# Optimization experiments

Measured on AMD Instinct MI355X. Metric: run time of the kernel, lower is better.

## Reference

```python
import jax, jax.numpy as jnp
import numpy as np


def setup_inputs() -> dict:
    key = jax.random.key(0)
    k1, k2 = jax.random.split(key)
    B, H, W, C = 32, 32, 32, 256
    N_EMBED = 1024
    z = jax.random.normal(k1, (B, H, W, C), dtype=jnp.float32)
    emb_weights = jax.random.normal(k2, (N_EMBED, C), dtype=jnp.float32)
    return {"z": z, "emb_weights": emb_weights}


def reference(z, emb_weights):
    # z: (B,H,W,C) -> flatten to (N, C)
    B = z.shape[0]
    C = z.shape[-1]
    z_flat = z.reshape(-1, C)  # (N, C)
    # Squared euclidean distance via ||z||^2 + ||e||^2 - 2 z.e^T
    distance = (
        jnp.sum(z_flat ** 2, axis=1, keepdims=True)          # (N, 1)
        + jnp.sum(emb_weights ** 2, axis=1)                   # (n_embed,)
        - 2.0 * jnp.dot(z_flat, emb_weights.T)                # (N, n_embed)
    )
    min_encoding_indices = jnp.argmin(distance, axis=1)       # (N,)
    z_q = emb_weights[min_encoding_indices].reshape(z.shape)  # (B,H,W,C)
    min_encoding_indices = min_encoding_indices.reshape(B, -1)
    return z_q, min_encoding_indices
```

## Files before the change

kernel.cpp:

```cpp
#include <hip/hip_runtime.h>

#define C_DIM 256
#define NCODE 1024
#define MARGIN 0.02f

typedef __bf16 bf16x8 __attribute__((ext_vector_type(8)));
typedef float f32x4 __attribute__((ext_vector_type(4)));

#define WS_ENORM 0
#define WS_META  4096
#define WS_RLIST 8192
#define WS_BP    139264
#define WS_PB    1187840
#define WS_PBI   1712128

#define GLOAD_LDS16(g, s)                                                            \
  __builtin_amdgcn_global_load_lds(                                                  \
      (const __attribute__((address_space(1))) unsigned int*)(g),                    \
      (__attribute__((address_space(3))) unsigned int*)(s), 16, 0, 0)

__device__ __forceinline__ void bf16split(float x, unsigned short& h, unsigned short& l) {
    unsigned u  = __float_as_uint(x);
    unsigned rh = (u + 0x7FFFu + ((u >> 16) & 1u)) & 0xFFFF0000u;
    float    lf = x - __uint_as_float(rh);
    unsigned ul = __float_as_uint(lf);
    h = (unsigned short)(rh >> 16);
    l = (unsigned short)((ul + 0x7FFFu + ((ul >> 16) & 1u)) >> 16);
}

__global__ __launch_bounds__(256) void prep_misc_kernel(const float* __restrict__ emb,
                                                        float* __restrict__ enorm,
                                                        unsigned* __restrict__ meta) {
    int gid = blockIdx.x * 256 + threadIdx.x;
    if (gid == 0) meta[0] = 0u;
    int row = gid >> 6, lane = gid & 63;
    float4 v = reinterpret_cast<const float4*>(emb)[(size_t)row * 64 + lane];
    float s = v.x * v.x + v.y * v.y + v.z * v.z + v.w * v.w;
    #pragma unroll
    for (int off = 32; off; off >>= 1) s += __shfl_xor(s, off, 64);
    if (lane == 0) enorm[row] = s;
}

__global__ __launch_bounds__(256) void prep_b_kernel(const float* __restrict__ emb,
                                                     unsigned short* __restrict__ bp) {
    int tid = blockIdx.x * 256 + threadIdx.x;
    int j   = tid >> 5;
    int u   = tid & 31;
    int kc  = u >> 2, lg = u & 3;
    const float* src = emb + (size_t)j * C_DIM + kc * 32 + lg * 8;
    float4 v0 = *reinterpret_cast<const float4*>(src);
    float4 v1 = *reinterpret_cast<const float4*>(src + 4);
    float vs[8] = {v0.x, v0.y, v0.z, v0.w, v1.x, v1.y, v1.z, v1.w};
    unsigned short h[8], l[8];
    #pragma unroll
    for (int k = 0; k < 8; ++k) bf16split(vs[k], h[k], l[k]);
    int chunk = j >> 5, nf = (j >> 4) & 1, lr = j & 15;
    int lane  = lg * 16 + lr;
    size_t base = (size_t)chunk * 16384 + (size_t)(nf * 8 + kc) * 512 + lane * 8;
    uint4 hp, lp;
    hp.x = (unsigned)h[0] | ((unsigned)h[1] << 16);
    hp.y = (unsigned)h[2] | ((unsigned)h[3] << 16);
    hp.z = (unsigned)h[4] | ((unsigned)h[5] << 16);
    hp.w = (unsigned)h[6] | ((unsigned)h[7] << 16);
    lp.x = (unsigned)l[0] | ((unsigned)l[1] << 16);
    lp.y = (unsigned)l[2] | ((unsigned)l[3] << 16);
    lp.z = (unsigned)l[4] | ((unsigned)l[5] << 16);
    lp.w = (unsigned)l[6] | ((unsigned)l[7] << 16);
    *reinterpret_cast<uint4*>(bp + base)             = hp;
    *reinterpret_cast<uint4*>(bp + base + 16 * 512)  = lp;
}

__global__ __launch_bounds__(512, 2) void vq_main_kernel(
    const float* __restrict__ z, const unsigned short* __restrict__ bp,
    const float* __restrict__ enorm, float2* __restrict__ pb,
    unsigned* __restrict__ pbi) {
    __shared__ alignas(16) unsigned short Bds[2][16384];
    __shared__ float en_s[512];
    __shared__ float mv1[128][2], mv2[128][2];
    __shared__ unsigned mi[128][2];

    const int t    = threadIdx.x;
    const int w    = t >> 6;
    const int lane = t & 63;
    const int lr   = lane & 15, lg = lane >> 4;
    const int wm   = w >> 1;
    const int ng   = w & 1;
    const int  nh  = blockIdx.x & 1;
    const long r0  = (long)(blockIdx.x >> 1) * 128;
    const unsigned short* bph = bp + (size_t)nh * 16 * 16384;

    #pragma unroll
    for (int round = 0; round < 4; ++round) {
        int f = round * 8 + w;
        GLOAD_LDS16(bph + (size_t)f * 512 + lane * 8, &Bds[0][f * 512]);
    }
    if (t < 512) en_s[t] = enorm[nh * 512 + t];

    bf16x8 ah[2][8], al[2][8];
    #pragma unroll
    for (int m = 0; m < 2; ++m) {
        const float* zr = z + (r0 + wm * 32 + m * 16 + lr) * C_DIM + lg * 8;
        #pragma unroll
        for (int kc = 0; kc < 8; ++kc) {
            float4 v0 = *reinterpret_cast<const float4*>(zr + kc * 32);
            float4 v1 = *reinterpret_cast<const float4*>(zr + kc * 32 + 4);
            float vs[8] = {v0.x, v0.y, v0.z, v0.w, v1.x, v1.y, v1.z, v1.w};
            unsigned short hv[8], lv[8];
            #pragma unroll
            for (int jj = 0; jj < 8; ++jj) bf16split(vs[jj], hv[jj], lv[jj]);
            unsigned hp[4] = {
                (unsigned)hv[0] | ((unsigned)hv[1] << 16), (unsigned)hv[2] | ((unsigned)hv[3] << 16),
                (unsigned)hv[4] | ((unsigned)hv[5] << 16), (unsigned)hv[6] | ((unsigned)hv[7] << 16)};
            unsigned lp[4] = {
                (unsigned)lv[0] | ((unsigned)lv[1] << 16), (unsigned)lv[2] | ((unsigned)lv[3] << 16),
                (unsigned)lv[4] | ((unsigned)lv[5] << 16), (unsigned)lv[6] | ((unsigned)lv[7] << 16)};
            ah[m][kc] = __builtin_bit_cast(bf16x8, *reinterpret_cast<uint4*>(hp));
            al[m][kc] = __builtin_bit_cast(bf16x8, *reinterpret_cast<uint4*>(lp));
        }
    }

    float b1[2][4], b2[2][4]; unsigned i1[2][4];
    #pragma unroll
    for (int m = 0; m < 2; ++m)
        #pragma unroll
        for (int r = 0; r < 4; ++r) { b1[m][r] = 3.4e38f; b2[m][r] = 3.4e38f; i1[m][r] = 0; }

    for (int c = 0; c < 16; ++c) {
        const int cur = c & 1;
        __syncthreads();
        if (c < 15) {
            const unsigned short* src = bph + (size_t)(c + 1) * 16384;
            #pragma unroll
            for (int round = 0; round < 4; ++round) {
                int f = round * 8 + w;
                GLOAD_LDS16(src + (size_t)f * 512 + lane * 8, &Bds[cur ^ 1][f * 512]);
            }
            asm volatile("s_waitcnt vmcnt(4)" ::: "memory");
        } else {
            asm volatile("s_waitcnt vmcnt(0)" ::: "memory");
        }
        __syncthreads();

        f32x4 hh0 = {0.f,0.f,0.f,0.f}, hh1 = {0.f,0.f,0.f,0.f};
        f32x4 hl0 = {0.f,0.f,0.f,0.f}, hl1 = {0.f,0.f,0.f,0.f};
        f32x4 lh0 = {0.f,0.f,0.f,0.f}, lh1 = {0.f,0.f,0.f,0.f};
        const unsigned short* bb = &Bds[cur][(ng * 8) * 512 + lane * 8];
        #pragma unroll
        for (int kc = 0; kc < 8; ++kc) {
            bf16x8 bh = *reinterpret_cast<const bf16x8*>(bb + kc * 512);
            bf16x8 bl = *reinterpret_cast<const bf16x8*>(bb + (16 + kc) * 512);
            hh0 = __builtin_amdgcn_mfma_f32_16x16x32_bf16(ah[0][kc], bh, hh0, 0, 0, 0);
            hh1 = __builtin_amdgcn_mfma_f32_16x16x32_bf16(ah[1][kc], bh, hh1, 0, 0, 0);
            lh0 = __builtin_amdgcn_mfma_f32_16x16x32_bf16(al[0][kc], bh, lh0, 0, 0, 0);
            lh1 = __builtin_amdgcn_mfma_f32_16x16x32_bf16(al[1][kc], bh, lh1, 0, 0, 0);
            hl0 = __builtin_amdgcn_mfma_f32_16x16x32_bf16(ah[0][kc], bl, hl0, 0, 0, 0);
            hl1 = __builtin_amdgcn_mfma_f32_16x16x32_bf16(ah[1][kc], bl, hl1, 0, 0, 0);
        }

        const float    en   = en_s[c * 32 + ng * 16 + lr];
        const unsigned code = (unsigned)(nh * 512 + c * 32 + ng * 16 + lr);
        #pragma unroll
        for (int r = 0; r < 4; ++r) {
            float d0 = fmaf(-2.f, hh0[r] + hl0[r] + lh0[r], en);
            if (d0 < b1[0][r]) { b2[0][r] = b1[0][r]; b1[0][r] = d0; i1[0][r] = code; }
            else if (d0 < b2[0][r]) { b2[0][r] = d0; }
            float d1 = fmaf(-2.f, hh1[r] + hl1[r] + lh1[r], en);
            if (d1 < b1[1][r]) { b2[1][r] = b1[1][r]; b1[1][r] = d1; i1[1][r] = code; }
            else if (d1 < b2[1][r]) { b2[1][r] = d1; }
        }
    }

    #pragma unroll
    for (int m = 0; m < 2; ++m)
        #pragma unroll
        for (int r = 0; r < 4; ++r) {
            float v1 = b1[m][r], v2 = b2[m][r]; unsigned j1 = i1[m][r];
            #pragma unroll
            for (int off = 8; off; off >>= 1) {
                float    ov1 = __shfl_xor(v1, off, 64);
                float    ov2 = __shfl_xor(v2, off, 64);
                unsigned oj1 = (unsigned)__shfl_xor((int)j1, off, 64);
                if (ov1 < v1 || (ov1 == v1 && oj1 < j1)) {
                    v2 = fminf(v1, ov2); v1 = ov1; j1 = oj1;
                } else {
                    v2 = fminf(v2, ov1);
                }
            }
            if (lr == 0) {
                int rowl = wm * 32 + m * 16 + lg * 4 + r;
                mv1[rowl][ng] = v1; mv2[rowl][ng] = v2; mi[rowl][ng] = j1;
            }
        }
    __syncthreads();
    if (t < 128) {
        float B1 = mv1[t][0], B2 = mv2[t][0]; unsigned I1 = mi[t][0];
        float o1 = mv1[t][1], o2 = mv2[t][1]; unsigned O1 = mi[t][1];
        if (o1 < B1 || (o1 == B1 && O1 < I1)) { B2 = fminf(B1, o2); B1 = o1; I1 = O1; }
        else                                  { B2 = fminf(B2, o1); }
        pb [(r0 + t) * 2 + nh] = make_float2(B1, B2);
        pbi[(r0 + t) * 2 + nh] = I1;
    }
}

__global__ __launch_bounds__(256) void finalize_gather_kernel(
    const float* __restrict__ emb, const float2* __restrict__ pb,
    const unsigned* __restrict__ pbi, float* __restrict__ zq,
    float* __restrict__ idx_out, unsigned* __restrict__ meta,
    unsigned* __restrict__ rlist) {
    const long row = (long)blockIdx.x * 4 + (threadIdx.x >> 6);
    const int lane = threadIdx.x & 63;
    float2   p0 = pb [row * 2 + 0], p1 = pb [row * 2 + 1];
    unsigned j0 = pbi[row * 2 + 0], j1 = pbi[row * 2 + 1];
    float B1, B2; unsigned I1;
    if (p1.x < p0.x) { B1 = p1.x; I1 = j1; B2 = fminf(p0.x, p1.y); }
    else             { B1 = p0.x; I1 = j0; B2 = fminf(p0.y, p1.x); }
    if (lane == 0) {
        idx_out[row] = (float)I1;
        if (B2 - B1 <= MARGIN) rlist[atomicAdd(meta, 1u)] = (unsigned)row;
    }
    float4 v = reinterpret_cast<const float4*>(emb)[(size_t)I1 * 64 + lane];
    reinterpret_cast<float4*>(zq)[row * 64 + lane] = v;
}

__global__ __launch_bounds__(256) void rescue_kernel(
    const float* __restrict__ z, const float* __restrict__ emb,
    const float* __restrict__ enorm, const unsigned* __restrict__ meta,
    const unsigned* __restrict__ rlist, float* __restrict__ zq,
    float* __restrict__ idx_out) {
    __shared__ float zrow[C_DIM];
    __shared__ float rd[256];
    __shared__ unsigned rix[256];
    const unsigned cnt = meta[0];
    for (unsigned li = blockIdx.x; li < cnt; li += gridDim.x) {
        unsigned row = rlist[li];
        __syncthreads();
        if (threadIdx.x < 64) {
            float4 v = reinterpret_cast<const float4*>(z)[(size_t)row * 64 + threadIdx.x];
            reinterpret_cast<float4*>(zrow)[threadIdx.x] = v;
        }
        __syncthreads();
        const int c = threadIdx.x;
        float a0 = 0.f, a1 = 0.f, a2 = 0.f, a3 = 0.f;
        const float4* zp = reinterpret_cast<const float4*>(zrow);
        const float4* e0 = reinterpret_cast<const float4*>(emb + (size_t)(c)       * C_DIM);
        const float4* e1 = reinterpret_cast<const float4*>(emb + (size_t)(c + 256) * C_DIM);
        const float4* e2 = reinterpret_cast<const float4*>(emb + (size_t)(c + 512) * C_DIM);
        const float4* e3 = reinterpret_cast<const float4*>(emb + (size_t)(c + 768) * C_DIM);
        #pragma unroll 8
        for (int k = 0; k < 64; ++k) {
            float4 z4 = zp[k];
            float4 f0 = e0[k], f1 = e1[k], f2 = e2[k], f3 = e3[k];
            a0 = fmaf(z4.x, f0.x, a0); a0 = fmaf(z4.y, f0.y, a0);
            a0 = fmaf(z4.z, f0.z, a0); a0 = fmaf(z4.w, f0.w, a0);
            a1 = fmaf(z4.x, f1.x, a1); a1 = fmaf(z4.y, f1.y, a1);
            a1 = fmaf(z4.z, f1.z, a1); a1 = fmaf(z4.w, f1.w, a1);
            a2 = fmaf(z4.x, f2.x, a2); a2 = fmaf(z4.y, f2.y, a2);
            a2 = fmaf(z4.z, f2.z, a2); a2 = fmaf(z4.w, f2.w, a2);
            a3 = fmaf(z4.x, f3.x, a3); a3 = fmaf(z4.y, f3.y, a3);
            a3 = fmaf(z4.z, f3.z, a3); a3 = fmaf(z4.w, f3.w, a3);
        }
        float d0 = fmaf(-2.f, a0, enorm[c]);
        float d1 = fmaf(-2.f, a1, enorm[c + 256]);
        float d2 = fmaf(-2.f, a2, enorm[c + 512]);
        float d3 = fmaf(-2.f, a3, enorm[c + 768]);
        float bd = d0; unsigned bi = (unsigned)c;
        if (d1 < bd) { bd = d1; bi = (unsigned)(c + 256); }
        if (d2 < bd) { bd = d2; bi = (unsigned)(c + 512); }
        if (d3 < bd) { bd = d3; bi = (unsigned)(c + 768); }
        rd[threadIdx.x] = bd; rix[threadIdx.x] = bi;
        __syncthreads();
        for (int s = 128; s; s >>= 1) {
            if (threadIdx.x < (unsigned)s) {
                float od = rd[threadIdx.x + s]; unsigned oi = rix[threadIdx.x + s];
                if (od < rd[threadIdx.x] ||
                    (od == rd[threadIdx.x] && oi < rix[threadIdx.x])) {
                    rd[threadIdx.x] = od; rix[threadIdx.x] = oi;
                }
            }
            __syncthreads();
        }
        unsigned code = rix[0];
        if (threadIdx.x < 64) {
            float4 v = reinterpret_cast<const float4*>(emb)[(size_t)code * 64 + threadIdx.x];
            reinterpret_cast<float4*>(zq)[(size_t)row * 64 + threadIdx.x] = v;
        }
        if (threadIdx.x == 0) idx_out[row] = (float)code;
    }
}

extern "C" void kernel_launch(void* const* d_in, const int* in_sizes, int n_in,
                              void* d_out, int out_size, void* d_ws, size_t ws_size,
                              hipStream_t stream) {
    const float* z   = (const float*)d_in[0];
    const float* emb = (const float*)d_in[1];
    const int n = in_sizes[0] / C_DIM;

    float* zq      = (float*)d_out;
    float* idx_out = zq + (size_t)n * C_DIM;

    char* ws = (char*)d_ws;
    float*          enorm = (float*)(ws + WS_ENORM);
    unsigned*       meta  = (unsigned*)(ws + WS_META);
    unsigned*       rlist = (unsigned*)(ws + WS_RLIST);
    unsigned short* bp    = (unsigned short*)(ws + WS_BP);
    float2*         pb    = (float2*)(ws + WS_PB);
    unsigned*       pbi   = (unsigned*)(ws + WS_PBI);

    prep_misc_kernel<<<256, 256, 0, stream>>>(emb, enorm, meta);
    prep_b_kernel<<<128, 256, 0, stream>>>(emb, bp);
    vq_main_kernel<<<(n / 128) * 2, 512, 0, stream>>>(z, bp, enorm, pb, pbi);
    finalize_gather_kernel<<<n / 4, 256, 0, stream>>>(emb, pb, pbi, zq, idx_out,
                                                      meta, rlist);
    rescue_kernel<<<256, 256, 0, stream>>>(z, emb, enorm, meta, rlist, zq, idx_out);
}
```

Baseline: 149.3 us.

## Split VQ search into bf16 coarse pass, split-bf16 refine pass, then fp32 rescue

The main pass now computes distances with a single bf16 MFMA product instead of the three-term hi/lo split, cutting MFMA work by about two thirds and halving B traffic. Each wave now owns all 32 codes of a chunk, and a 4-deep prefetch ring replaces double buffering. Rows whose top-two gap falls under a wider margin are re-scored over all codes by a new stage-2 kernel that uses the split-bf16 precision. Rows that remain ambiguous go to the existing fp32 rescue kernel. The risk is that the wider margin sends many rows to stage 2 and adds a kernel launch.

Result: slower. 219.2 us (+46.9%).

```diff
diff --git a/kernel.cpp b/kernel.cpp
--- a/kernel.cpp
+++ b/kernel.cpp
@@ -2,37 +2,44 @@
 
 #define C_DIM 256
 #define NCODE 1024
-#define MARGIN 0.02f
+#define MARGIN1 0.35f
+#define MARGIN2 0.02f
 
 typedef __bf16 bf16x8 __attribute__((ext_vector_type(8)));
 typedef float f32x4 __attribute__((ext_vector_type(4)));
 
-#define WS_ENORM 0
-#define WS_META  4096
-#define WS_RLIST 8192
-#define WS_BP    139264
-#define WS_PB    1187840
-#define WS_PBI   1712128
+#define WS_ENORM  0
+#define WS_META   4096
+#define WS_RLIST  8192
+#define WS_RLIST2 139264
+#define WS_BP     270336
+#define WS_PB     1318912
+#define WS_PBI    1843200
+
+#define BP_LO_OFF 262144
 
 #define GLOAD_LDS16(g, s)                                                            \
   __builtin_amdgcn_global_load_lds(                                                  \
       (const __attribute__((address_space(1))) unsigned int*)(g),                    \
       (__attribute__((address_space(3))) unsigned int*)(s), 16, 0, 0)
 
+__device__ __forceinline__ unsigned short bf16rne(float x) {
+    unsigned u = __float_as_uint(x);
+    return (unsigned short)((u + 0x7FFFu + ((u >> 16) & 1u)) >> 16);
+}
 __device__ __forceinline__ void bf16split(float x, unsigned short& h, unsigned short& l) {
     unsigned u  = __float_as_uint(x);
     unsigned rh = (u + 0x7FFFu + ((u >> 16) & 1u)) & 0xFFFF0000u;
     float    lf = x - __uint_as_float(rh);
-    unsigned ul = __float_as_uint(lf);
     h = (unsigned short)(rh >> 16);
-    l = (unsigned short)((ul + 0x7FFFu + ((ul >> 16) & 1u)) >> 16);
+    l = bf16rne(lf);
 }
 
 __global__ __launch_bounds__(256) void prep_misc_kernel(const float* __restrict__ emb,
                                                         float* __restrict__ enorm,
                                                         unsigned* __restrict__ meta) {
     int gid = blockIdx.x * 256 + threadIdx.x;
-    if (gid == 0) meta[0] = 0u;
+    if (gid < 2) meta[gid] = 0u;
     int row = gid >> 6, lane = gid & 63;
     float4 v = reinterpret_cast<const float4*>(emb)[(size_t)row * 64 + lane];
     float s = v.x * v.x + v.y * v.y + v.z * v.z + v.w * v.w;
@@ -56,7 +63,7 @@
     for (int k = 0; k < 8; ++k) bf16split(vs[k], h[k], l[k]);
     int chunk = j >> 5, nf = (j >> 4) & 1, lr = j & 15;
     int lane  = lg * 16 + lr;
-    size_t base = (size_t)chunk * 16384 + (size_t)(nf * 8 + kc) * 512 + lane * 8;
+    size_t base = (size_t)chunk * 8192 + (size_t)(nf * 8 + kc) * 512 + lane * 8;
     uint4 hp, lp;
     hp.x = (unsigned)h[0] | ((unsigned)h[1] << 16);
     hp.y = (unsigned)h[2] | ((unsigned)h[3] << 16);
@@ -67,57 +74,53 @@
     lp.z = (unsigned)l[4] | ((unsigned)l[5] << 16);
     lp.w = (unsigned)l[6] | ((unsigned)l[7] << 16);
     *reinterpret_cast<uint4*>(bp + base)             = hp;
-    *reinterpret_cast<uint4*>(bp + base + 16 * 512)  = lp;
-}
-
-__global__ __launch_bounds__(512, 2) void vq_main_kernel(
+    *reinterpret_cast<uint4*>(bp + BP_LO_OFF + base) = lp;
+}
+
+__global__ __launch_bounds__(256, 2) void vq_stage1_kernel(
     const float* __restrict__ z, const unsigned short* __restrict__ bp,
     const float* __restrict__ enorm, float2* __restrict__ pb,
     unsigned* __restrict__ pbi) {
-    __shared__ alignas(16) unsigned short Bds[2][16384];
+    __shared__ unsigned short Bds[4][8192];
     __shared__ float en_s[512];
-    __shared__ float mv1[128][2], mv2[128][2];
-    __shared__ unsigned mi[128][2];
-
-    const int t    = threadIdx.x;
-    const int w    = t >> 6;
-    const int lane = t & 63;
-    const int lr   = lane & 15, lg = lane >> 4;
-    const int wm   = w >> 1;
-    const int ng   = w & 1;
-    const int  nh  = blockIdx.x & 1;
-    const long r0  = (long)(blockIdx.x >> 1) * 128;
-    const unsigned short* bph = bp + (size_t)nh * 16 * 16384;
-
-    #pragma unroll
-    for (int round = 0; round < 4; ++round) {
-        int f = round * 8 + w;
-        GLOAD_LDS16(bph + (size_t)f * 512 + lane * 8, &Bds[0][f * 512]);
-    }
-    if (t < 512) en_s[t] = enorm[nh * 512 + t];
-
-    bf16x8 ah[2][8], al[2][8];
+
+    const int t = threadIdx.x;
+    const int w = t >> 6, lane = t & 63;
+    const int lr = lane & 15, lg = lane >> 4;
+    const int nh = blockIdx.x & 1;
+    const long r0 = (long)(blockIdx.x >> 1) * 128 + w * 32;
+    const unsigned short* bsrc = bp + (size_t)(nh * 16) * 8192 + lane * 8;
+
+    en_s[t]       = enorm[nh * 512 + t];
+    en_s[t + 256] = enorm[nh * 512 + 256 + t];
+
+    bf16x8 ah[2][8];
     #pragma unroll
     for (int m = 0; m < 2; ++m) {
-        const float* zr = z + (r0 + wm * 32 + m * 16 + lr) * C_DIM + lg * 8;
+        const float* zr = z + (r0 + m * 16 + lr) * C_DIM + lg * 8;
         #pragma unroll
         for (int kc = 0; kc < 8; ++kc) {
             float4 v0 = *reinterpret_cast<const float4*>(zr + kc * 32);
             float4 v1 = *reinterpret_cast<const float4*>(zr + kc * 32 + 4);
             float vs[8] = {v0.x, v0.y, v0.z, v0.w, v1.x, v1.y, v1.z, v1.w};
-            unsigned short hv[8], lv[8];
-            #pragma unroll
-            for (int jj = 0; jj < 8; ++jj) bf16split(vs[jj], hv[jj], lv[jj]);
-            unsigned hp[4] = {
-                (unsigned)hv[0] | ((unsigned)hv[1] << 16), (unsigned)hv[2] | ((unsigned)hv[3] << 16),
-                (unsigned)hv[4] | ((unsigned)hv[5] << 16), (unsigned)hv[6] | ((unsigned)hv[7] << 16)};
-            unsigned lp[4] = {
-                (unsigned)lv[0] | ((unsigned)lv[1] << 16), (unsigned)lv[2] | ((unsigned)lv[3] << 16),
-                (unsigned)lv[4] | ((unsigned)lv[5] << 16), (unsigned)lv[6] | ((unsigned)lv[7] << 16)};
+            unsigned hp[4];
+            #pragma unroll
+            for (int p = 0; p < 4; ++p)
+                hp[p] = (unsigned)bf16rne(vs[2 * p]) |
+                        ((unsigned)bf16rne(vs[2 * p + 1]) << 16);
             ah[m][kc] = __builtin_bit_cast(bf16x8, *reinterpret_cast<uint4*>(hp));
-            al[m][kc] = __builtin_bit_cast(bf16x8, *reinterpret_cast<uint4*>(lp));
         }
     }
+    __syncthreads();
+
+#define STG1(c) {                                                       \
+    unsigned short* db = &Bds[(c) & 3][0];                              \
+    const unsigned short* gs = bsrc + (size_t)(c) * 8192;               \
+    _Pragma("unroll") for (int rd = 0; rd < 4; ++rd) {                  \
+        int s_ = rd * 4 + w;                                            \
+        GLOAD_LDS16(gs + s_ * 512, db + s_ * 512); } }
+
+    STG1(0); STG1(1); STG1(2);
 
     float b1[2][4], b2[2][4]; unsigned i1[2][4];
     #pragma unroll
@@ -125,50 +128,47 @@
         #pragma unroll
         for (int r = 0; r < 4; ++r) { b1[m][r] = 3.4e38f; b2[m][r] = 3.4e38f; i1[m][r] = 0; }
 
+    #pragma unroll 1
     for (int c = 0; c < 16; ++c) {
-        const int cur = c & 1;
-        __syncthreads();
-        if (c < 15) {
-            const unsigned short* src = bph + (size_t)(c + 1) * 16384;
-            #pragma unroll
-            for (int round = 0; round < 4; ++round) {
-                int f = round * 8 + w;
-                GLOAD_LDS16(src + (size_t)f * 512 + lane * 8, &Bds[cur ^ 1][f * 512]);
-            }
-            asm volatile("s_waitcnt vmcnt(4)" ::: "memory");
-        } else {
-            asm volatile("s_waitcnt vmcnt(0)" ::: "memory");
-        }
-        __syncthreads();
-
-        f32x4 hh0 = {0.f,0.f,0.f,0.f}, hh1 = {0.f,0.f,0.f,0.f};
-        f32x4 hl0 = {0.f,0.f,0.f,0.f}, hl1 = {0.f,0.f,0.f,0.f};
-        f32x4 lh0 = {0.f,0.f,0.f,0.f}, lh1 = {0.f,0.f,0.f,0.f};
-        const unsigned short* bb = &Bds[cur][(ng * 8) * 512 + lane * 8];
+        if (c < 13) {
+            STG1(c + 3);
+            asm volatile("s_waitcnt vmcnt(12)" ::: "memory");
+        } else if (c == 13) { asm volatile("s_waitcnt vmcnt(8)" ::: "memory"); }
+        else if (c == 14)   { asm volatile("s_waitcnt vmcnt(4)" ::: "memory"); }
+        else                { asm volatile("s_waitcnt vmcnt(0)" ::: "memory"); }
+        __builtin_amdgcn_s_barrier();
+
+        f32x4 a00 = {0.f,0.f,0.f,0.f}, a01 = {0.f,0.f,0.f,0.f};
+        f32x4 a10 = {0.f,0.f,0.f,0.f}, a11 = {0.f,0.f,0.f,0.f};
+        const unsigned short* bb = &Bds[c & 3][lane * 8];
         #pragma unroll
         for (int kc = 0; kc < 8; ++kc) {
-            bf16x8 bh = *reinterpret_cast<const bf16x8*>(bb + kc * 512);
-            bf16x8 bl = *reinterpret_cast<const bf16x8*>(bb + (16 + kc) * 512);
-            hh0 = __builtin_amdgcn_mfma_f32_16x16x32_bf16(ah[0][kc], bh, hh0, 0, 0, 0);
-            hh1 = __builtin_amdgcn_mfma_f32_16x16x32_bf16(ah[1][kc], bh, hh1, 0, 0, 0);
-            lh0 = __builtin_amdgcn_mfma_f32_16x16x32_bf16(al[0][kc], bh, lh0, 0, 0, 0);
-            lh1 = __builtin_amdgcn_mfma_f32_16x16x32_bf16(al[1][kc], bh, lh1, 0, 0, 0);
-            hl0 = __builtin_amdgcn_mfma_f32_16x16x32_bf16(ah[0][kc], bl, hl0, 0, 0, 0);
-            hl1 = __builtin_amdgcn_mfma_f32_16x16x32_bf16(ah[1][kc], bl, hl1, 0, 0, 0);
-        }
-
-        const float    en   = en_s[c * 32 + ng * 16 + lr];
-        const unsigned code = (unsigned)(nh * 512 + c * 32 + ng * 16 + lr);
-        #pragma unroll
-        for (int r = 0; r < 4; ++r) {
-            float d0 = fmaf(-2.f, hh0[r] + hl0[r] + lh0[r], en);
-            if (d0 < b1[0][r]) { b2[0][r] = b1[0][r]; b1[0][r] = d0; i1[0][r] = code; }
-            else if (d0 < b2[0][r]) { b2[0][r] = d0; }
-            float d1 = fmaf(-2.f, hh1[r] + hl1[r] + lh1[r], en);
-            if (d1 < b1[1][r]) { b2[1][r] = b1[1][r]; b1[1][r] = d1; i1[1][r] = code; }
-            else if (d1 < b2[1][r]) { b2[1][r] = d1; }
-        }
+            bf16x8 bh0 = *reinterpret_cast<const bf16x8*>(bb + kc * 512);
+            bf16x8 bh1 = *reinterpret_cast<const bf16x8*>(bb + (8 + kc) * 512);
+            a00 = __builtin_amdgcn_mfma_f32_16x16x32_bf16(ah[0][kc], bh0, a00, 0, 0, 0);
+            a10 = __builtin_amdgcn_mfma_f32_16x16x32_bf16(ah[1][kc], bh0, a10, 0, 0, 0);
+            a01 = __builtin_amdgcn_mfma_f32_16x16x32_bf16(ah[0][kc], bh1, a01, 0, 0, 0);
+            a11 = __builtin_amdgcn_mfma_f32_16x16x32_bf16(ah[1][kc], bh1, a11, 0, 0, 0);
+        }
+
+        #pragma unroll
+        for (int nf = 0; nf < 2; ++nf) {
+            const int cl = c * 32 + nf * 16 + lr;
+            const float en = en_s[cl];
+            const unsigned code = (unsigned)(nh * 512 + cl);
+            #pragma unroll
+            for (int r = 0; r < 4; ++r) {
+                float d0 = fmaf(-2.f, (nf ? a01[r] : a00[r]), en);
+                if (d0 < b1[0][r]) { b2[0][r] = b1[0][r]; b1[0][r] = d0; i1[0][r] = code; }
+                else if (d0 < b2[0][r]) { b2[0][r] = d0; }
+                float d1 = fmaf(-2.f, (nf ? a11[r] : a10[r]), en);
+                if (d1 < b1[1][r]) { b2[1][r] = b1[1][r]; b1[1][r] = d1; i1[1][r] = code; }
+                else if (d1 < b2[1][r]) { b2[1][r] = d1; }
+            }
+        }
+        __builtin_amdgcn_s_barrier();
     }
+#undef STG1
 
     #pragma unroll
     for (int m = 0; m < 2; ++m)
@@ -187,19 +187,11 @@
                 }
             }
             if (lr == 0) {
-                int rowl = wm * 32 + m * 16 + lg * 4 + r;
-                mv1[rowl][ng] = v1; mv2[rowl][ng] = v2; mi[rowl][ng] = j1;
-            }
-        }
-    __syncthreads();
-    if (t < 128) {
-        float B1 = mv1[t][0], B2 = mv2[t][0]; unsigned I1 = mi[t][0];
-        float o1 = mv1[t][1], o2 = mv2[t][1]; unsigned O1 = mi[t][1];
-        if (o1 < B1 || (o1 == B1 && O1 < I1)) { B2 = fminf(B1, o2); B1 = o1; I1 = O1; }
-        else                                  { B2 = fminf(B2, o1); }
-        pb [(r0 + t) * 2 + nh] = make_float2(B1, B2);
-        pbi[(r0 + t) * 2 + nh] = I1;
-    }
+                long row = r0 + m * 16 + lg * 4 + r;
+                pb [row * 2 + nh] = make_float2(v1, v2);
+                pbi[row * 2 + nh] = j1;
+            }
+        }
 }
 
 __global__ __launch_bounds__(256) void finalize_gather_kernel(
@@ -216,23 +208,146 @@
     else             { B1 = p0.x; I1 = j0; B2 = fminf(p0.y, p1.x); }
     if (lane == 0) {
         idx_out[row] = (float)I1;
-        if (B2 - B1 <= MARGIN) rlist[atomicAdd(meta, 1u)] = (unsigned)row;
+        if (B2 - B1 <= MARGIN1) rlist[atomicAdd(meta, 1u)] = (unsigned)row;
     }
     float4 v = reinterpret_cast<const float4*>(emb)[(size_t)I1 * 64 + lane];
     reinterpret_cast<float4*>(zq)[row * 64 + lane] = v;
 }
 
+__global__ __launch_bounds__(256) void vq_stage2_kernel(
+    const float* __restrict__ z, const unsigned short* __restrict__ bp,
+    const float* __restrict__ enorm, const float* __restrict__ emb,
+    const unsigned* __restrict__ meta, const unsigned* __restrict__ rlist,
+    float* __restrict__ zq, float* __restrict__ idx_out,
+    unsigned* __restrict__ meta2, unsigned* __restrict__ rlist2) {
+    __shared__ float en_s[NCODE];
+    __shared__ unsigned rows_w[4][16];
+    __shared__ unsigned codes_w[4][16];
+    const int t = threadIdx.x, w = t >> 6, lane = t & 63;
+    const int lr = lane & 15, lg = lane >> 4;
+    en_s[t] = enorm[t]; en_s[t + 256] = enorm[t + 256];
+    en_s[t + 512] = enorm[t + 512]; en_s[t + 768] = enorm[t + 768];
+    __syncthreads();
+    const unsigned cnt = meta[0];
+    const unsigned wid = blockIdx.x * 4 + (unsigned)w;
+    const unsigned stride = gridDim.x * 64;
+
+    for (unsigned base = wid * 16; base < cnt; base += stride) {
+        unsigned slot = base + (unsigned)lr;
+        unsigned row = rlist[slot < cnt ? slot : 0];
+        bf16x8 ah[8], al[8];
+        const float* zr = z + (size_t)row * C_DIM + lg * 8;
+        #pragma unroll
+        for (int kc = 0; kc < 8; ++kc) {
+            float4 v0 = *reinterpret_cast<const float4*>(zr + kc * 32);
+            float4 v1 = *reinterpret_cast<const float4*>(zr + kc * 32 + 4);
+            float vs[8] = {v0.x, v0.y, v0.z, v0.w, v1.x, v1.y, v1.z, v1.w};
+            unsigned short hv[8], lv[8];
+            #pragma unroll
+            for (int jj = 0; jj < 8; ++jj) bf16split(vs[jj], hv[jj], lv[jj]);
+            unsigned hp[4] = {
+                (unsigned)hv[0] | ((unsigned)hv[1] << 16), (unsigned)hv[2] | ((unsigned)hv[3] << 16),
+                (unsigned)hv[4] | ((unsigned)hv[5] << 16), (unsigned)hv[6] | ((unsigned)hv[7] << 16)};
+            unsigned lp[4] = {
+                (unsigned)lv[0] | ((unsigned)lv[1] << 16), (unsigned)lv[2] | ((unsigned)lv[3] << 16),
+                (unsigned)lv[4] | ((unsigned)lv[5] << 16), (unsigned)lv[6] | ((unsigned)lv[7] << 16)};
+            ah[kc] = __builtin_bit_cast(bf16x8, *reinterpret_cast<uint4*>(hp));
+            al[kc] = __builtin_bit_cast(bf16x8, *reinterpret_cast<uint4*>(lp));
+        }
+
+        float b1[4], b2[4]; unsigned i1[4];
+        #pragma unroll
+        for (int r = 0; r < 4; ++r) { b1[r] = 3.4e38f; b2[r] = 3.4e38f; i1[r] = 0; }
+
+        for (int c = 0; c < 32; ++c) {
+            f32x4 hh0 = {0.f,0.f,0.f,0.f}, hh1 = {0.f,0.f,0.f,0.f};
+            f32x4 hl0 = {0.f,0.f,0.f,0.f}, hl1 = {0.f,0.f,0.f,0.f};
+            f32x4 lh0 = {0.f,0.f,0.f,0.f}, lh1 = {0.f,0.f,0.f,0.f};
+            const unsigned short* cb = bp + (size_t)c * 8192 + lane * 8;
+            #pragma unroll
+            for (int kc = 0; kc < 8; ++kc) {
+                bf16x8 bh0 = *reinterpret_cast<const bf16x8*>(cb + kc * 512);
+                bf16x8 bh1 = *reinterpret_cast<const bf16x8*>(cb + (8 + kc) * 512);
+                bf16x8 bl0 = *reinterpret_cast<const bf16x8*>(cb + BP_LO_OFF + kc * 512);
+                bf16x8 bl1 = *reinterpret_cast<const bf16x8*>(cb + BP_LO_OFF + (8 + kc) * 512);
+                hh0 = __builtin_amdgcn_mfma_f32_16x16x32_bf16(ah[kc], bh0, hh0, 0, 0, 0);
+                hh1 = __builtin_amdgcn_mfma_f32_16x16x32_bf16(ah[kc], bh1, hh1, 0, 0, 0);
+                lh0 = __builtin_amdgcn_mfma_f32_16x16x32_bf16(al[kc], bh0, lh0, 0, 0, 0);
+                lh1 = __builtin_amdgcn_mfma_f32_16x16x32_bf16(al[kc], bh1, lh1, 0, 0, 0);
+                hl0 = __builtin_amdgcn_mfma_f32_16x16x32_bf16(ah[kc], bl0, hl0, 0, 0, 0);
+                hl1 = __builtin_amdgcn_mfma_f32_16x16x32_bf16(ah[kc], bl1, hl1, 0, 0, 0);
+            }
+            #pragma unroll
+            for (int nf = 0; nf < 2; ++nf) {
+                const unsigned code = (unsigned)(c * 32 + nf * 16 + lr);
+                const float en = en_s[code];
+                #pragma unroll
+                for (int r = 0; r < 4; ++r) {
+                    float s3 = nf ? (hh1[r] + hl1[r] + lh1[r]) : (hh0[r] + hl0[r] + lh0[r]);
+                    float d = fmaf(-2.f, s3, en);
+                    if (d < b1[r]) { b2[r] = b1[r]; b1[r] = d; i1[r] = code; }
+                    else if (d < b2[r]) { b2[r] = d; }
+                }
+            }
+        }
+
+        #pragma unroll
+        for (int r = 0; r < 4; ++r) {
+            float v1 = b1[r], v2 = b2[r]; unsigned j1 = i1[r];
+            #pragma unroll
+            for (int off = 8; off; off >>= 1) {
+                float    ov1 = __shfl_xor(v1, off, 64);
+                float    ov2 = __shfl_xor(v2, off, 64);
+                unsigned oj1 = (unsigned)__shfl_xor((int)j1, off, 64);
+                if (ov1 < v1 || (ov1 == v1 && oj1 < j1)) {
+                    v2 = fminf(v1, ov2); v1 = ov1; j1 = oj1;
+                } else {
+                    v2 = fminf(v2, ov1);
+                }
+            }
+            b1[r] = v1; b2[r] = v2; i1[r] = j1;
+        }
+        if (lr == 0) {
+            #pragma unroll
+            for (int r = 0; r < 4; ++r) {
+                int rs = lg * 4 + r;
+                unsigned sl = base + (unsigned)rs;
+                if (sl < cnt) {
+                    unsigned rrow = rlist[sl];
+                    rows_w[w][rs]  = rrow;
+                    codes_w[w][rs] = i1[r];
+                    idx_out[rrow]  = (float)i1[r];
+                    if (b2[r] - b1[r] <= MARGIN2) rlist2[atomicAdd(meta2, 1u)] = rrow;
+                } else {
+                    rows_w[w][rs] = 0xFFFFFFFFu;
+                }
+            }
+        }
+        {
+            int rr = lane >> 2, q = lane & 3;
+            unsigned rrow = rows_w[w][rr];
+            if (rrow != 0xFFFFFFFFu) {
+                unsigned code = codes_w[w][rr];
+                const float4* ep = reinterpret_cast<const float4*>(emb) + (size_t)code * 64 + q * 16;
+                float4*       op = reinterpret_cast<float4*>(zq) + (size_t)rrow * 64 + q * 16;
+                #pragma unroll
+                for (int j2 = 0; j2 < 16; ++j2) op[j2] = ep[j2];
+            }
+        }
+    }
+}
+
 __global__ __launch_bounds__(256) void rescue_kernel(
     const float* __restrict__ z, const float* __restrict__ emb,
-    const float* __restrict__ enorm, const unsigned* __restrict__ meta,
-    const unsigned* __restrict__ rlist, float* __restrict__ zq,
+    const float* __restrict__ enorm, const unsigned* __restrict__ meta2,
+    const unsigned* __restrict__ rlist2, float* __restrict__ zq,
     float* __restrict__ idx_out) {
     __shared__ float zrow[C_DIM];
     __shared__ float rd[256];
     __shared__ unsigned rix[256];
-    const unsigned cnt = meta[0];
+    const unsigned cnt = meta2[0];
     for (unsigned li = blockIdx.x; li < cnt; li += gridDim.x) {
-        unsigned row = rlist[li];
+        unsigned row = rlist2[li];
         __syncthreads();
         if (threadIdx.x < 64) {
             float4 v = reinterpret_cast<const float4*>(z)[(size_t)row * 64 + threadIdx.x];
@@ -299,17 +414,21 @@
     float* idx_out = zq + (size_t)n * C_DIM;
 
     char* ws = (char*)d_ws;
-    float*          enorm = (float*)(ws + WS_ENORM);
-    unsigned*       meta  = (unsigned*)(ws + WS_META);
-    unsigned*       rlist = (unsigned*)(ws + WS_RLIST);
-    unsigned short* bp    = (unsigned short*)(ws + WS_BP);
-    float2*         pb    = (float2*)(ws + WS_PB);
-    unsigned*       pbi   = (unsigned*)(ws + WS_PBI);
+    float*          enorm  = (float*)(ws + WS_ENORM);
+    unsigned*       meta   = (unsigned*)(ws + WS_META);
+    unsigned*       rlist  = (unsigned*)(ws + WS_RLIST);
+    unsigned*       rlist2 = (unsigned*)(ws + WS_RLIST2);
+    unsigned short* bp     = (unsigned short*)(ws + WS_BP);
+    float2*         pb     = (float2*)(ws + WS_PB);
+    unsigned*       pbi    = (unsigned*)(ws + WS_PBI);
 
     prep_misc_kernel<<<256, 256, 0, stream>>>(emb, enorm, meta);
     prep_b_kernel<<<128, 256, 0, stream>>>(emb, bp);
-    vq_main_kernel<<<(n / 128) * 2, 512, 0, stream>>>(z, bp, enorm, pb, pbi);
+    vq_stage1_kernel<<<(n / 128) * 2, 256, 0, stream>>>(z, bp, enorm, pb, pbi);
     finalize_gather_kernel<<<n / 4, 256, 0, stream>>>(emb, pb, pbi, zq, idx_out,
                                                       meta, rlist);
-    rescue_kernel<<<256, 256, 0, stream>>>(z, emb, enorm, meta, rlist, zq, idx_out);
-}
+    vq_stage2_kernel<<<256, 256, 0, stream>>>(z, bp, enorm, emb, meta, rlist,
+                                              zq, idx_out, meta + 1, rlist2);
+    rescue_kernel<<<256, 256, 0, stream>>>(z, emb, enorm, meta + 1, rlist2,
+                                           zq, idx_out);
+}
```
